# Performance work log

Hardware: AMD Instinct MI355X
Metric: run time of the kernel (lower is better)

## Reference

```python
import jax, jax.numpy as jnp
import numpy as np

INPUT_SIZE = 32768
MINICOL_SIZE = 8
NUM_MINICOLS = INPUT_SIZE // MINICOL_SIZE  # 4096
SYN_PERM_CONNECTED = 0.1
NUM_ACTIVE = 82  # num_active_columns_per_inhibition_area


def setup_inputs() -> dict:
    key = jax.random.key(0)
    k1, k2 = jax.random.split(key)
    input_vector = (jax.random.uniform(k1, (INPUT_SIZE,)) < 0.05).astype(jnp.float32)
    # connections: rand binarized at syn_perm_connected, per initialize_connections().
    connections = (jax.random.uniform(k2, (NUM_MINICOLS, INPUT_SIZE)) >= SYN_PERM_CONNECTED
                   ).astype(jnp.float32)
    boosting_factors = jnp.ones((NUM_MINICOLS,), dtype=jnp.float32)
    return {"input_vector": input_vector, "connections": connections,
            "boosting_factors": boosting_factors}


def reference(input_vector, connections, boosting_factors):
    # compute_overlap: per-minicolumn masked sum == matvec over binary mask.
    overlap = jnp.einsum("ci,i->c", connections, input_vector)  # [C]
    boosted = overlap * boosting_factors                         # [C]
    # global_inhibition_func: top-k winners -> binary active-column SDR.
    _, winners = jax.lax.top_k(boosted, NUM_ACTIVE)
    active_columns = jnp.zeros((NUM_MINICOLS,), dtype=boosted.dtype).at[winners].set(1.0)
    # Return active mask and the masked boosted overlap (winner activations).
    return active_columns, active_columns * boosted
```

## Files before the change

kernel.cpp:

```cpp
#include <hip/hip_runtime.h>

#define INPUT_SIZE 32768
#define NUM_COLS   4096
#define NUM_ACTIVE 82

__global__ __launch_bounds__(256) void matvec_boost_kernel(
    const float* __restrict__ conn, const float* __restrict__ input,
    const float* __restrict__ boost, float* __restrict__ overlap)
{
    const int c = blockIdx.x;
    const int t = threadIdx.x;
    const float4* row = (const float4*)(conn + (size_t)c * INPUT_SIZE);
    const float4* in4 = (const float4*)input;

    float acc0 = 0.f, acc1 = 0.f;
    #pragma unroll
    for (int k = 0; k < INPUT_SIZE / 4 / 256; k += 2) {
        float4 a0 = row[t + 256 * k];
        float4 b0 = in4[t + 256 * k];
        float4 a1 = row[t + 256 * (k + 1)];
        float4 b1 = in4[t + 256 * (k + 1)];
        acc0 += a0.x * b0.x + a0.y * b0.y + a0.z * b0.z + a0.w * b0.w;
        acc1 += a1.x * b1.x + a1.y * b1.y + a1.z * b1.z + a1.w * b1.w;
    }
    float acc = acc0 + acc1;

    #pragma unroll
    for (int off = 32; off > 0; off >>= 1)
        acc += __shfl_down(acc, off, 64);

    __shared__ float part[4];
    const int wave = t >> 6;
    if ((t & 63) == 0) part[wave] = acc;
    __syncthreads();
    if (t == 0) {
        float tot = part[0] + part[1] + part[2] + part[3];
        overlap[c] = tot * boost[c];
    }
}

__global__ __launch_bounds__(64) void topk_mask_kernel(
    const float* __restrict__ vals, float* __restrict__ out)
{
    const int c = blockIdx.x;
    const int lane = threadIdx.x;
    const float v = vals[c];
    const float4* v4 = (const float4*)vals;

    int cnt = 0;
    #pragma unroll
    for (int k = 0; k < NUM_COLS / 4 / 64; ++k) {
        const int i4 = lane + 64 * k;
        float4 b = v4[i4];
        const int j = i4 * 4;
        cnt += (b.x > v) || (b.x == v && (j + 0) < c);
        cnt += (b.y > v) || (b.y == v && (j + 1) < c);
        cnt += (b.z > v) || (b.z == v && (j + 2) < c);
        cnt += (b.w > v) || (b.w == v && (j + 3) < c);
    }
    #pragma unroll
    for (int off = 32; off > 0; off >>= 1)
        cnt += __shfl_down(cnt, off, 64);

    if (lane == 0) {
        const bool act = cnt < NUM_ACTIVE;
        out[c] = act ? 1.0f : 0.0f;
        out[NUM_COLS + c] = act ? v : 0.0f;
    }
}

extern "C" void kernel_launch(void* const* d_in, const int* in_sizes, int n_in,
                              void* d_out, int out_size, void* d_ws, size_t ws_size,
                              hipStream_t stream) {
    const float* input = (const float*)d_in[0];
    const float* conn  = (const float*)d_in[1];
    const float* boost = (const float*)d_in[2];
    float* out = (float*)d_out;
    float* ov  = (float*)d_ws;

    matvec_boost_kernel<<<NUM_COLS, 256, 0, stream>>>(conn, input, boost, ov);
    topk_mask_kernel<<<NUM_COLS, 64, 0, stream>>>(ov, out);
}
```

Measured before the change: 675.8 us.

## Process four matrix rows per block with nontemporal loads in matvec

The matvec kernel now has each block compute four rows, so every load of the input vector is reused across four rows and the grid shrinks by a factor of four. The connection matrix is read with nontemporal loads so the single-use streaming data does not pollute the caches. More loads are in flight per thread, which raises register use, and the smaller grid may reduce how much latency the hardware can hide.

```diff
diff --git a/kernel.cpp b/kernel.cpp
--- a/kernel.cpp
+++ b/kernel.cpp
@@ -3,39 +3,66 @@
 #define INPUT_SIZE 32768
 #define NUM_COLS   4096
 #define NUM_ACTIVE 82
+#define ROWS_PER_BLOCK 4
+#define NF4 (INPUT_SIZE / 4)
+
+typedef float v4f __attribute__((ext_vector_type(4)));
+
+__device__ __forceinline__ float dot4(v4f a, v4f b) {
+    return a.x * b.x + a.y * b.y + a.z * b.z + a.w * b.w;
+}
 
 __global__ __launch_bounds__(256) void matvec_boost_kernel(
     const float* __restrict__ conn, const float* __restrict__ input,
     const float* __restrict__ boost, float* __restrict__ overlap)
 {
-    const int c = blockIdx.x;
-    const int t = threadIdx.x;
-    const float4* row = (const float4*)(conn + (size_t)c * INPUT_SIZE);
-    const float4* in4 = (const float4*)input;
+    const int r0 = blockIdx.x * ROWS_PER_BLOCK;
+    const int t  = threadIdx.x;
+    const v4f* in4 = (const v4f*)input;
+    const v4f* row0 = (const v4f*)(conn + (size_t)(r0 + 0) * INPUT_SIZE);
+    const v4f* row1 = (const v4f*)(conn + (size_t)(r0 + 1) * INPUT_SIZE);
+    const v4f* row2 = (const v4f*)(conn + (size_t)(r0 + 2) * INPUT_SIZE);
+    const v4f* row3 = (const v4f*)(conn + (size_t)(r0 + 3) * INPUT_SIZE);
 
-    float acc0 = 0.f, acc1 = 0.f;
-    #pragma unroll
-    for (int k = 0; k < INPUT_SIZE / 4 / 256; k += 2) {
-        float4 a0 = row[t + 256 * k];
-        float4 b0 = in4[t + 256 * k];
-        float4 a1 = row[t + 256 * (k + 1)];
-        float4 b1 = in4[t + 256 * (k + 1)];
-        acc0 += a0.x * b0.x + a0.y * b0.y + a0.z * b0.z + a0.w * b0.w;
-        acc1 += a1.x * b1.x + a1.y * b1.y + a1.z * b1.z + a1.w * b1.w;
+    float acc[ROWS_PER_BLOCK] = {0.f, 0.f, 0.f, 0.f};
+
+    for (int k = t; k < NF4; k += 512) {
+        const int k2 = k + 256;
+        v4f b0 = in4[k];
+        v4f b1 = in4[k2];
+        v4f a00 = __builtin_nontemporal_load(&row0[k]);
+        v4f a01 = __builtin_nontemporal_load(&row0[k2]);
+        v4f a10 = __builtin_nontemporal_load(&row1[k]);
+        v4f a11 = __builtin_nontemporal_load(&row1[k2]);
+        v4f a20 = __builtin_nontemporal_load(&row2[k]);
+        v4f a21 = __builtin_nontemporal_load(&row2[k2]);
+        v4f a30 = __builtin_nontemporal_load(&row3[k]);
+        v4f a31 = __builtin_nontemporal_load(&row3[k2]);
+        acc[0] += dot4(a00, b0) + dot4(a01, b1);
+        acc[1] += dot4(a10, b0) + dot4(a11, b1);
+        acc[2] += dot4(a20, b0) + dot4(a21, b1);
+        acc[3] += dot4(a30, b0) + dot4(a31, b1);
     }
-    float acc = acc0 + acc1;
 
     #pragma unroll
-    for (int off = 32; off > 0; off >>= 1)
-        acc += __shfl_down(acc, off, 64);
+    for (int r = 0; r < ROWS_PER_BLOCK; ++r) {
+        float a = acc[r];
+        #pragma unroll
+        for (int off = 32; off > 0; off >>= 1)
+            a += __shfl_down(a, off, 64);
+        acc[r] = a;
+    }
 
-    __shared__ float part[4];
+    __shared__ float part[4][ROWS_PER_BLOCK];
     const int wave = t >> 6;
-    if ((t & 63) == 0) part[wave] = acc;
+    if ((t & 63) == 0) {
+        #pragma unroll
+        for (int r = 0; r < ROWS_PER_BLOCK; ++r) part[wave][r] = acc[r];
+    }
     __syncthreads();
-    if (t == 0) {
-        float tot = part[0] + part[1] + part[2] + part[3];
-        overlap[c] = tot * boost[c];
+    if (t < ROWS_PER_BLOCK) {
+        float tot = part[0][t] + part[1][t] + part[2][t] + part[3][t];
+        overlap[r0 + t] = tot * boost[r0 + t];
     }
 }
 
@@ -78,6 +105,6 @@
     float* out = (float*)d_out;
     float* ov  = (float*)d_ws;
 
-    matvec_boost_kernel<<<NUM_COLS, 256, 0, stream>>>(conn, input, boost, ov);
+    matvec_boost_kernel<<<NUM_COLS / ROWS_PER_BLOCK, 256, 0, stream>>>(conn, input, boost, ov);
     topk_mask_kernel<<<NUM_COLS, 64, 0, stream>>>(ov, out);
 }
```

After: 649.9 us. 3.8% less time.
